# Performance work log

Hardware: AMD Instinct MI355X
Metric: run time of the kernel (lower is better)

## Reference

```python
import jax, jax.numpy as jnp
import numpy as np
from jax import lax

# dims: T timesteps, CIN=6 DoG channels, HxW image; F conv filters, K kernel
T, CIN, H, W_IN = 15, 6, 512, 512
F, K, PAD = 64, 5, 2
THRESH = 15.0
K_WTA, RADIUS = 5, 2  # self.k1, self.r1


def setup_inputs() -> dict:
    key = jax.random.key(0)
    k1, k2 = jax.random.split(key)
    # cumulative binary spike wave: once a unit spikes it stays 1 (SpykeTorch convention)
    ev = (jax.random.uniform(k1, (T, CIN, H, W_IN)) < 0.02).astype(jnp.float32)
    x = jnp.clip(jnp.cumsum(ev, axis=0), 0.0, 1.0)
    w = 0.8 + 0.05 * jax.random.normal(k2, (F, CIN, K, K), dtype=jnp.float32)
    return {"x": x, "w": w}


def _pool_pad(x, pad):
    # sf.pooling(x, 2, 2): max-pool 2x2 stride 2; sf.pad: zero pad
    x = lax.reduce_window(x, -jnp.inf, lax.max, (1, 1, 2, 2), (1, 1, 2, 2), 'VALID')
    return jnp.pad(x, ((0, 0), (0, 0), (pad, pad), (pad, pad)))


def _fire(pot, thr):
    # sf.fire(pot, thr, True): zero sub-threshold potentials, spikes = sign
    tp = jnp.where(pot < thr, 0.0, pot)
    return jnp.sign(tp), tp


def _pointwise_inhibition(pot):
    # keep, per spatial site, only the feature with the earliest (then strongest) spike
    T_ = pot.shape[0]
    max_vals = jnp.max(pot, axis=1, keepdims=True)      # [T,1,H,W]
    max_idx = jnp.argmax(pot, axis=1, keepdims=True)    # [T,1,H,W]
    clamp = jnp.sign(max_vals)                          # 1 where any feature active
    earliest = jnp.clip(T_ - jnp.sum(clamp, axis=0, keepdims=True), 0, T_ - 1).astype(jnp.int32)  # [1,1,H,W]
    winners = jnp.take_along_axis(max_idx, earliest, axis=0)  # [1,1,H,W] winning feature
    has_spike = clamp[-1:]                              # [1,1,H,W] any spike by last step
    ch = jnp.arange(pot.shape[1]).reshape(1, -1, 1, 1)
    coef = jnp.where(ch == winners, has_spike, 0.0)     # scatter of winner coeff
    return pot * coef


def _get_k_winners(pot, spikes, k, radius):
    # NMS-like radius-based k-winners-take-all over [F,H,W]
    T_ = pot.shape[0]
    earliest = jnp.clip(T_ - jnp.sum(spikes, axis=0, keepdims=True), 0, T_ - 1).astype(jnp.int32)
    values = jnp.take_along_axis(pot, earliest, axis=0)  # potential at earliest spike
    trunc = spikes * values
    v = jnp.max(trunc) * T_  # large bias favoring earlier spikes
    total = jnp.sum(trunc + spikes * v, axis=0)          # [F,H,W]
    Fc, Hh, Ww = total.shape
    feat = jnp.arange(Fc).reshape(-1, 1, 1)
    row = jnp.arange(Hh).reshape(1, -1, 1)
    col = jnp.arange(Ww).reshape(1, 1, -1)
    winners = []
    for _ in range(k):  # small fixed k (5), fine to unroll
        idx = jnp.argmax(total)
        val = jnp.reshape(total, (-1,))[idx]
        f, r, c = jnp.unravel_index(idx, total.shape)
        active = val != 0
        win = jnp.where(active, jnp.stack([f, r, c]).astype(jnp.int32),
                        jnp.full((3,), -1, jnp.int32))
        winners.append(win)
        suppress = (feat == f) | ((jnp.abs(row - r) <= radius) & (jnp.abs(col - c) <= radius))
        total = jnp.where(active & suppress, 0.0, total)
    return jnp.stack(winners)  # [k,3] with -1 rows when fewer winners exist


def reference(x, w):
    inp = _pool_pad(x, PAD)  # [T,6,260,260]
    pot = lax.conv_general_dilated(inp, w, (1, 1), 'VALID',
                                   dimension_numbers=('NCHW', 'OIHW', 'NCHW'))  # [T,F,256,256]
    spk, pot = _fire(pot, THRESH)
    pot = _pointwise_inhibition(pot)
    spk = jnp.sign(pot)
    winners = _get_k_winners(pot, spk, K_WTA, RADIUS)
    return spk, winners
```

## Files before the change

### kernel.cpp

```cpp
#include <hip/hip_runtime.h>
#include <hip/hip_bf16.h>

#define T_ 15
#define CIN_ 6
#define F_ 64
#define HW_ 256
#define PW_ 260
#define THRESH_ 15.0f
#define TAU_NEVER 15


__global__ __launch_bounds__(256) void pool_tau(const float* __restrict__ x,
                                                unsigned char* __restrict__ tau,
                                                unsigned long long* __restrict__ slots,
                                                unsigned int* __restrict__ gmaxp,
                                                unsigned int* __restrict__ donep) {
    int idx = blockIdx.x * 256 + threadIdx.x;
    if (idx < 5) slots[idx] = 0ULL;
    if (idx == 5) *gmaxp = 0u;
    if (idx == 6) *donep = 0u;
    if (idx >= CIN_ * PW_ * PW_) return;
    int xx = idx % PW_;
    int rest = idx / PW_;
    int yy = rest % PW_;
    int c = rest / PW_;
    unsigned char tv = TAU_NEVER;
    if (xx >= 2 && xx < 258 && yy >= 2 && yy < 258) {
        int i = yy - 2, j = xx - 2;
        const float* b0 = x + ((size_t)c * 512 + 2 * i) * 512 + 2 * j;
        const size_t tstride = (size_t)CIN_ * 512 * 512;
        {
            const float* b = b0 + 14 * tstride;
            float2 a = *(const float2*)b;
            float2 d = *(const float2*)(b + 512);
            if (a.x > 0.f || a.y > 0.f || d.x > 0.f || d.y > 0.f) {
                int lo = 0, hi = 14;
                while (lo < hi) {
                    int mid = (lo + hi) >> 1;
                    const float* bm = b0 + (size_t)mid * tstride;
                    float2 am = *(const float2*)bm;
                    float2 dm = *(const float2*)(bm + 512);
                    bool on = (am.x > 0.f || am.y > 0.f || dm.x > 0.f || dm.y > 0.f);
                    if (on) hi = mid; else lo = mid + 1;
                }
                tv = (unsigned char)lo;
            }
        }
    }
    tau[idx] = tv;
}

__global__ __launch_bounds__(256, 3) void phaseA(const unsigned char* __restrict__ tau,
                                                 const float* __restrict__ w,
                                                 int* __restrict__ rec_wch,
                                                 float* __restrict__ rec_val,
                                                 int* __restrict__ rec_e,
                                                 unsigned int* __restrict__ gmaxp) {
    __shared__ float wl2[150 * 64];
    __shared__ unsigned char tw[CIN_ * 144];
    __shared__ float wmax[4];

    const int tid = threadIdx.x;
    const int lane = tid & 63;
    const int g = tid >> 6;
    const int gx = (g & 1) * 4;
    const int gy = (g >> 1) * 4;
    const int px0 = blockIdx.x * 8;
    const int py0 = blockIdx.y * 8;

    for (int idx = tid; idx < 9600; idx += 256) {
        int k = idx >> 6, f = idx & 63;
        wl2[idx] = w[f * 150 + k];
    }
    for (int idx = tid; idx < CIN_ * 144; idx += 256) {
        int c = idx / 144;
        int rem = idx - c * 144;
        int r = rem / 12;
        int xx = rem - r * 12;
        tw[idx] = tau[(c * PW_ + (py0 + r)) * PW_ + (px0 + xx)];
    }
    __syncthreads();

    unsigned int done = 0;
    int myw = -1, mye = T_;
    float myv = 0.0f;
    float wavemax = 0.0f;

    for (int t = 0; t < T_; ++t) {
        float acc[16];
#pragma unroll
        for (int i = 0; i < 16; ++i) acc[i] = 0.0f;

        for (int c = 0; c < CIN_; ++c) {
            float win[8][8];
            const unsigned char* tb = &tw[c * 144 + gy * 12 + gx];
#pragma unroll
            for (int r = 0; r < 8; ++r) {
                unsigned int lo = *(const unsigned int*)(tb + r * 12);
                unsigned int hi = *(const unsigned int*)(tb + r * 12 + 4);
#pragma unroll
                for (int b = 0; b < 4; ++b) {
                    win[r][b]     = (((lo >> (8 * b)) & 0xFF) <= (unsigned)t) ? 1.0f : 0.0f;
                    win[r][4 + b] = (((hi >> (8 * b)) & 0xFF) <= (unsigned)t) ? 1.0f : 0.0f;
                }
            }
#pragma unroll
            for (int ki = 0; ki < 5; ++ki)
#pragma unroll
                for (int kj = 0; kj < 5; ++kj) {
                    float wv = wl2[((c * 25 + ki * 5 + kj) << 6) + lane];
#pragma unroll
                    for (int py = 0; py < 4; ++py)
#pragma unroll
                        for (int px = 0; px < 4; ++px)
                            acc[py * 4 + px] += win[py + ki][px + kj] * wv;
                }
        }

#pragma unroll
        for (int i = 0; i < 16; ++i) {
            if (done & (1u << i)) continue;
            float v = acc[i];
            v = (v < THRESH_) ? 0.0f : v;
            if (__any(v > 0.0f)) {
                unsigned long long key =
                    ((unsigned long long)__float_as_uint(v) << 6) | (unsigned)(63 - lane);
#pragma unroll
                for (int m = 1; m < 64; m <<= 1) {
                    unsigned long long o = __shfl_xor(key, m, 64);
                    if (o > key) key = o;
                }
                float mv = __uint_as_float((unsigned int)(key >> 6));
                int wf = 63 - (int)(key & 63ULL);
                done |= (1u << i);
                if (lane == i) { myw = wf; myv = mv; mye = t; }
                wavemax = fmaxf(wavemax, mv);
            }
        }
        if (done == 0xFFFFu) break;
    }

    if (lane < 16) {
        int py = lane >> 2, px = lane & 3;
        int p = (py0 + gy + py) * HW_ + (px0 + gx + px);
        rec_wch[p] = myw;
        rec_val[p] = myv;
        rec_e[p] = mye;
    }
    if (lane == 0) wmax[g] = wavemax;
    __syncthreads();
    if (tid == 0) {
        float m = fmaxf(fmaxf(wmax[0], wmax[1]), fmaxf(wmax[2], wmax[3]));
        if (m > 0.0f) atomicMax(gmaxp, __float_as_uint(m));
    }
}

__global__ __launch_bounds__(256) void render(const int* __restrict__ rec_wch,
                                              const int* __restrict__ rec_e,
                                              float* __restrict__ out) {
    const int tid = threadIdx.x;
    const int t = blockIdx.y;
    const int fbase = blockIdx.z * 16;
    const int px = blockIdx.x * 1024 + tid * 4;

    int4 wch4 = *(const int4*)(rec_wch + px);
    int4 e4   = *(const int4*)(rec_e + px);
    int s0 = (wch4.x >= 0 && t >= e4.x) ? wch4.x : -1;
    int s1 = (wch4.y >= 0 && t >= e4.y) ? wch4.y : -1;
    int s2 = (wch4.z >= 0 && t >= e4.z) ? wch4.z : -1;
    int s3 = (wch4.w >= 0 && t >= e4.w) ? wch4.w : -1;

    float* base = out + (((size_t)t * F_ + fbase) << 16) + px;
#pragma unroll
    for (int fi = 0; fi < 16; ++fi) {
        int f = fbase + fi;
        float4 v;
        v.x = (f == s0) ? 1.0f : 0.0f;
        v.y = (f == s1) ? 1.0f : 0.0f;
        v.z = (f == s2) ? 1.0f : 0.0f;
        v.w = (f == s3) ? 1.0f : 0.0f;
        *(float4*)(base + ((size_t)fi << 16)) = v;
    }
}

__global__ __launch_bounds__(256) void max_round(const int* __restrict__ rec_wch,
                                                 const float* __restrict__ rec_val,
                                                 const int* __restrict__ rec_e,
                                                 const unsigned int* __restrict__ gmaxp,
                                                 unsigned long long* __restrict__ slots,
                                                 unsigned int* __restrict__ donep,
                                                 float* __restrict__ out,
                                                 int round) {
    __shared__ unsigned long long sred[256];
    int i = blockIdx.x * 256 + threadIdx.x;
    int fch = rec_wch[i];
    unsigned long long key = 0ULL;
    if (fch >= 0) {
        int e = rec_e[i];
        float base = rec_val[i] + 15.0f * __uint_as_float(*gmaxp);
        float tot = 0.0f;
        for (int t = e; t < T_; ++t) tot += base;
        if (tot > 0.0f) {
            int r = i >> 8, c = i & 255;
            bool sup = false;
            for (int j = 0; j < round; ++j) {
                unsigned long long s = slots[j];
                if (s == 0ULL) continue;
                int fl = 0x7fffffff - (int)(unsigned int)(s & 0xffffffffu);
                int fj = fl >> 16, rj = (fl >> 8) & 255, cj = fl & 255;
                int dr = r - rj; if (dr < 0) dr = -dr;
                int dc = c - cj; if (dc < 0) dc = -dc;
                if (fch == fj || (dr <= 2 && dc <= 2)) sup = true;
            }
            if (!sup) {
                int fl = (fch << 16) | i;
                unsigned int comp = 0x7fffffffu - (unsigned int)fl;
                key = ((unsigned long long)__float_as_uint(tot) << 32) | comp;
            }
        }
    }
    sred[threadIdx.x] = key;
    __syncthreads();
    for (int s = 128; s > 0; s >>= 1) {
        if (threadIdx.x < s) {
            if (sred[threadIdx.x + s] > sred[threadIdx.x]) sred[threadIdx.x] = sred[threadIdx.x + s];
        }
        __syncthreads();
    }
    if (threadIdx.x == 0) {
        if (sred[0] != 0ULL) atomicMax(&slots[round], sred[0]);
        if (round == 4) {
            __threadfence();
            unsigned int ticket = atomicAdd(donep, 1u);
            if (ticket == gridDim.x - 1) {
                float* wout = out + (size_t)T_ * F_ * HW_ * HW_;
                for (int r = 0; r < 5; ++r) {
                    unsigned long long s = atomicAdd(&slots[r], 0ULL);
                    if (s != 0ULL) {
                        int fl = 0x7fffffff - (int)(unsigned int)(s & 0xffffffffu);
                        wout[r * 3 + 0] = (float)(fl >> 16);
                        wout[r * 3 + 1] = (float)((fl >> 8) & 255);
                        wout[r * 3 + 2] = (float)(fl & 255);
                    } else {
                        wout[r * 3 + 0] = -1.0f; wout[r * 3 + 1] = -1.0f; wout[r * 3 + 2] = -1.0f;
                    }
                }
            }
        }
    }
}

extern "C" void kernel_launch(void* const* d_in, const int* in_sizes, int n_in,
                              void* d_out, int out_size, void* d_ws, size_t ws_size,
                              hipStream_t stream) {
    const float* x = (const float*)d_in[0];
    const float* w = (const float*)d_in[1];
    float* out = (float*)d_out;

    char* wsc = (char*)d_ws;
    unsigned char* tau = (unsigned char*)wsc;
    size_t off = (size_t)CIN_ * PW_ * PW_;
    int* rec_wch = (int*)(wsc + off);        off += 65536 * sizeof(int);
    float* rec_val = (float*)(wsc + off);    off += 65536 * sizeof(float);
    int* rec_e = (int*)(wsc + off);          off += 65536 * sizeof(int);
    unsigned long long* slots = (unsigned long long*)(wsc + off);  off += 8 * sizeof(unsigned long long);
    unsigned int* gmaxp = (unsigned int*)(wsc + off);  off += sizeof(unsigned int);
    unsigned int* donep = (unsigned int*)(wsc + off);

    pool_tau<<<(CIN_ * PW_ * PW_ + 255) / 256, 256, 0, stream>>>(x, tau, slots, gmaxp, donep);
    phaseA<<<dim3(32, 32), 256, 0, stream>>>(tau, w, rec_wch, rec_val, rec_e, gmaxp);
    render<<<dim3(64, 15, 4), 256, 0, stream>>>(rec_wch, rec_e, out);
    for (int r = 0; r < 5; ++r)
        max_round<<<256, 256, 0, stream>>>(rec_wch, rec_val, rec_e, gmaxp, slots, donep, out, r);
}
```

Before: 476.2 us.

## Skip provably sub-threshold timesteps in conv and fuse k-WTA rounds with grid barrier

phaseA computes, for each output pixel, an upper bound on its potential from the maximum weight times the cumulative count of active inputs. It then skips timesteps where no pixel in the wave can reach threshold, and exits early for pixels that never can. The five k-WTA max-reduction launches are merged into one persistent kernel that syncs rounds through global atomic counters and a spin barrier. That barrier assumes all 256 blocks are co-resident. The bound assumes the 15.0 threshold is only reachable with positive weights, which holds for these inputs.

```diff
diff --git a/kernel.cpp b/kernel.cpp
--- a/kernel.cpp
+++ b/kernel.cpp
@@ -1,5 +1,4 @@
 #include <hip/hip_runtime.h>
-#include <hip/hip_bf16.h>
 
 #define T_ 15
 #define CIN_ 6
@@ -14,11 +13,11 @@
                                                 unsigned char* __restrict__ tau,
                                                 unsigned long long* __restrict__ slots,
                                                 unsigned int* __restrict__ gmaxp,
-                                                unsigned int* __restrict__ donep) {
+                                                unsigned int* __restrict__ syncc) {
     int idx = blockIdx.x * 256 + threadIdx.x;
     if (idx < 5) slots[idx] = 0ULL;
     if (idx == 5) *gmaxp = 0u;
-    if (idx == 6) *donep = 0u;
+    if (idx >= 6 && idx < 11) syncc[idx - 6] = 0u;
     if (idx >= CIN_ * PW_ * PW_) return;
     int xx = idx % PW_;
     int rest = idx / PW_;
@@ -68,10 +67,17 @@
     const int px0 = blockIdx.x * 8;
     const int py0 = blockIdx.y * 8;
 
+    float wlocal = 0.0f;
     for (int idx = tid; idx < 9600; idx += 256) {
         int k = idx >> 6, f = idx & 63;
-        wl2[idx] = w[f * 150 + k];
-    }
+        float v = w[f * 150 + k];
+        wl2[idx] = v;
+        wlocal = fmaxf(wlocal, v);
+    }
+#pragma unroll
+    for (int m = 1; m < 64; m <<= 1)
+        wlocal = fmaxf(wlocal, __shfl_xor(wlocal, m, 64));
+    if (lane == 0) wmax[g] = wlocal;
     for (int idx = tid; idx < CIN_ * 144; idx += 256) {
         int c = idx / 144;
         int rem = idx - c * 144;
@@ -80,6 +86,37 @@
         tw[idx] = tau[(c * PW_ + (py0 + r)) * PW_ + (px0 + xx)];
     }
     __syncthreads();
+    const float wm = fmaxf(fmaxf(wmax[0], wmax[1]), fmaxf(wmax[2], wmax[3]));
+
+    int tmin = 15;
+    if (lane < 16) {
+        int py = lane >> 2, px = lane & 3;
+        unsigned int cnt0 = 0, cnt1 = 0, cnt2 = 0, cnt3 = 0;
+        for (int c = 0; c < CIN_; ++c) {
+            const unsigned char* tb = &tw[c * 144 + (gy + py) * 12 + (gx + px)];
+#pragma unroll
+            for (int ki = 0; ki < 5; ++ki)
+#pragma unroll
+                for (int kj = 0; kj < 5; ++kj) {
+                    unsigned int v = tb[ki * 12 + kj];
+                    unsigned int inc = 1u << ((v & 3u) * 8u);
+                    unsigned int wsel = v >> 2;
+                    cnt0 += (wsel == 0u) ? inc : 0u;
+                    cnt1 += (wsel == 1u) ? inc : 0u;
+                    cnt2 += (wsel == 2u) ? inc : 0u;
+                    cnt3 += (wsel == 3u) ? inc : 0u;
+                }
+        }
+        int run = 0;
+#pragma unroll
+        for (int t = 0; t < T_; ++t) {
+            unsigned int cw = (t < 4) ? cnt0 : (t < 8) ? cnt1 : (t < 12) ? cnt2 : cnt3;
+            run += (int)((cw >> ((t & 3) * 8)) & 0xFFu);
+            if (tmin == 15 && wm * (float)run >= 14.999f) tmin = t;
+        }
+    }
+    const unsigned int never =
+        (unsigned int)(__ballot(lane < 16 && tmin > 14) & 0xFFFFull);
 
     unsigned int done = 0;
     int myw = -1, mye = T_;
@@ -87,6 +124,13 @@
     float wavemax = 0.0f;
 
     for (int t = 0; t < T_; ++t) {
+        unsigned int cand =
+            (unsigned int)(__ballot(lane < 16 && t >= tmin) & 0xFFFFull) & ~done;
+        if (!cand) {
+            if ((done | never) == 0xFFFFu) break;
+            continue;
+        }
+
         float acc[16];
 #pragma unroll
         for (int i = 0; i < 16; ++i) acc[i] = 0.0f;
@@ -119,7 +163,7 @@
 
 #pragma unroll
         for (int i = 0; i < 16; ++i) {
-            if (done & (1u << i)) continue;
+            if (!(cand & (1u << i))) continue;
             float v = acc[i];
             v = (v < THRESH_) ? 0.0f : v;
             if (__any(v > 0.0f)) {
@@ -137,7 +181,7 @@
                 wavemax = fmaxf(wavemax, mv);
             }
         }
-        if (done == 0xFFFFu) break;
+        if ((done | never) == 0xFFFFu) break;
     }
 
     if (lane < 16) {
@@ -183,69 +227,74 @@
     }
 }
 
-__global__ __launch_bounds__(256) void max_round(const int* __restrict__ rec_wch,
-                                                 const float* __restrict__ rec_val,
-                                                 const int* __restrict__ rec_e,
-                                                 const unsigned int* __restrict__ gmaxp,
-                                                 unsigned long long* __restrict__ slots,
-                                                 unsigned int* __restrict__ donep,
-                                                 float* __restrict__ out,
-                                                 int round) {
+__global__ __launch_bounds__(256) void kwta(const int* __restrict__ rec_wch,
+                                            const float* __restrict__ rec_val,
+                                            const int* __restrict__ rec_e,
+                                            const unsigned int* __restrict__ gmaxp,
+                                            unsigned long long* __restrict__ slots,
+                                            unsigned int* __restrict__ syncc,
+                                            float* __restrict__ out) {
     __shared__ unsigned long long sred[256];
-    int i = blockIdx.x * 256 + threadIdx.x;
+    __shared__ unsigned long long swin;
+    const int tid = threadIdx.x;
+    const int i = blockIdx.x * 256 + tid;
+
     int fch = rec_wch[i];
-    unsigned long long key = 0ULL;
+    float tot = 0.0f;
     if (fch >= 0) {
         int e = rec_e[i];
         float base = rec_val[i] + 15.0f * __uint_as_float(*gmaxp);
-        float tot = 0.0f;
         for (int t = e; t < T_; ++t) tot += base;
-        if (tot > 0.0f) {
-            int r = i >> 8, c = i & 255;
-            bool sup = false;
-            for (int j = 0; j < round; ++j) {
-                unsigned long long s = slots[j];
-                if (s == 0ULL) continue;
-                int fl = 0x7fffffff - (int)(unsigned int)(s & 0xffffffffu);
-                int fj = fl >> 16, rj = (fl >> 8) & 255, cj = fl & 255;
-                int dr = r - rj; if (dr < 0) dr = -dr;
-                int dc = c - cj; if (dc < 0) dc = -dc;
-                if (fch == fj || (dr <= 2 && dc <= 2)) sup = true;
+    }
+    bool alive = (fch >= 0) && (tot > 0.0f);
+    unsigned long long mykey = 0ULL;
+    if (alive) {
+        unsigned int comp = 0x7fffffffu - (unsigned int)((fch << 16) | i);
+        mykey = ((unsigned long long)__float_as_uint(tot) << 32) | comp;
+    }
+    const int rr = i >> 8, cc = i & 255;
+    int wf[5], wr[5], wc[5];
+
+#pragma unroll
+    for (int round = 0; round < 5; ++round) {
+        sred[tid] = alive ? mykey : 0ULL;
+        __syncthreads();
+        for (int s = 128; s > 0; s >>= 1) {
+            if (tid < s) {
+                if (sred[tid + s] > sred[tid]) sred[tid] = sred[tid + s];
             }
-            if (!sup) {
-                int fl = (fch << 16) | i;
-                unsigned int comp = 0x7fffffffu - (unsigned int)fl;
-                key = ((unsigned long long)__float_as_uint(tot) << 32) | comp;
-            }
-        }
-    }
-    sred[threadIdx.x] = key;
-    __syncthreads();
-    for (int s = 128; s > 0; s >>= 1) {
-        if (threadIdx.x < s) {
-            if (sred[threadIdx.x + s] > sred[threadIdx.x]) sred[threadIdx.x] = sred[threadIdx.x + s];
+            __syncthreads();
+        }
+        if (tid == 0) {
+            if (sred[0] != 0ULL) atomicMax(&slots[round], sred[0]);
+            __threadfence();
+            atomicAdd(&syncc[round], 1u);
+            while (atomicAdd(&syncc[round], 0u) < gridDim.x)
+                __builtin_amdgcn_s_sleep(8);
+            __threadfence();
+            swin = atomicAdd(&slots[round], 0ULL);
         }
         __syncthreads();
-    }
-    if (threadIdx.x == 0) {
-        if (sred[0] != 0ULL) atomicMax(&slots[round], sred[0]);
-        if (round == 4) {
-            __threadfence();
-            unsigned int ticket = atomicAdd(donep, 1u);
-            if (ticket == gridDim.x - 1) {
-                float* wout = out + (size_t)T_ * F_ * HW_ * HW_;
-                for (int r = 0; r < 5; ++r) {
-                    unsigned long long s = atomicAdd(&slots[r], 0ULL);
-                    if (s != 0ULL) {
-                        int fl = 0x7fffffff - (int)(unsigned int)(s & 0xffffffffu);
-                        wout[r * 3 + 0] = (float)(fl >> 16);
-                        wout[r * 3 + 1] = (float)((fl >> 8) & 255);
-                        wout[r * 3 + 2] = (float)(fl & 255);
-                    } else {
-                        wout[r * 3 + 0] = -1.0f; wout[r * 3 + 1] = -1.0f; wout[r * 3 + 2] = -1.0f;
-                    }
-                }
-            }
+        unsigned long long s = swin;
+        if (s != 0ULL) {
+            int fl = 0x7fffffff - (int)(unsigned int)(s & 0xffffffffu);
+            int fj = fl >> 16, rj = (fl >> 8) & 255, cj = fl & 255;
+            wf[round] = fj; wr[round] = rj; wc[round] = cj;
+            int dr = rr - rj; if (dr < 0) dr = -dr;
+            int dc = cc - cj; if (dc < 0) dc = -dc;
+            if (fch == fj || (dr <= 2 && dc <= 2)) alive = false;
+        } else {
+            wf[round] = -1; wr[round] = -1; wc[round] = -1;
+        }
+    }
+
+    if (blockIdx.x == 0 && tid == 0) {
+        float* wout = out + (size_t)T_ * F_ * HW_ * HW_;
+#pragma unroll
+        for (int r = 0; r < 5; ++r) {
+            wout[r * 3 + 0] = (float)wf[r];
+            wout[r * 3 + 1] = (float)wr[r];
+            wout[r * 3 + 2] = (float)wc[r];
         }
     }
 }
@@ -263,13 +312,12 @@
     int* rec_wch = (int*)(wsc + off);        off += 65536 * sizeof(int);
     float* rec_val = (float*)(wsc + off);    off += 65536 * sizeof(float);
     int* rec_e = (int*)(wsc + off);          off += 65536 * sizeof(int);
-    unsigned long long* slots = (unsigned long long*)(wsc + off);  off += 8 * sizeof(unsigned long long);
+    unsigned long long* slots = (unsigned long long*)(wsc + off);  off += 5 * sizeof(unsigned long long);
     unsigned int* gmaxp = (unsigned int*)(wsc + off);  off += sizeof(unsigned int);
-    unsigned int* donep = (unsigned int*)(wsc + off);
-
-    pool_tau<<<(CIN_ * PW_ * PW_ + 255) / 256, 256, 0, stream>>>(x, tau, slots, gmaxp, donep);
+    unsigned int* syncc = (unsigned int*)(wsc + off);
+
+    pool_tau<<<(CIN_ * PW_ * PW_ + 255) / 256, 256, 0, stream>>>(x, tau, slots, gmaxp, syncc);
     phaseA<<<dim3(32, 32), 256, 0, stream>>>(tau, w, rec_wch, rec_val, rec_e, gmaxp);
     render<<<dim3(64, 15, 4), 256, 0, stream>>>(rec_wch, rec_e, out);
-    for (int r = 0; r < 5; ++r)
-        max_round<<<256, 256, 0, stream>>>(rec_wch, rec_val, rec_e, gmaxp, slots, donep, out, r);
-}
+    kwta<<<256, 256, 0, stream>>>(rec_wch, rec_val, rec_e, gmaxp, slots, syncc, out);
+}
```

After: 531.8 us. 1.12x slower.
